# Kernel tuning notes

Measured on AMD Instinct MI355X. Metric: run time of the kernel, lower is better.

The kernel has to match this reference:

```python
import jax, jax.numpy as jnp
import numpy as np

K = 8   # heads
d = 8   # per-head dim
D = K * d  # 64


def setup_inputs() -> dict:
    key = jax.random.key(0)
    ks = jax.random.split(key, 12)
    B, T, N = 8, 12, 512
    s2 = 1.0 / np.sqrt(2 * D)
    s1 = 1.0 / np.sqrt(D)
    return {
        "X": jax.random.normal(ks[0], (B, T, N, D), jnp.float32),
        "STE": jax.random.normal(ks[1], (B, T, N, D), jnp.float32),
        "W7": jax.random.uniform(ks[2], (2 * D, D), jnp.float32, -s2, s2),
        "b7": jnp.zeros((D,), jnp.float32),
        "W8": jax.random.uniform(ks[3], (2 * D, D), jnp.float32, -s2, s2),
        "b8": jnp.zeros((D,), jnp.float32),
        "W9": jax.random.uniform(ks[4], (2 * D, D), jnp.float32, -s2, s2),
        "b9": jnp.zeros((D,), jnp.float32),
        "W10": jax.random.uniform(ks[5], (D, D), jnp.float32, -s1, s1),
        "b10": jnp.zeros((D,), jnp.float32),
        "W11": jax.random.uniform(ks[6], (D, D), jnp.float32, -s1, s1),
        "b11": jnp.zeros((D,), jnp.float32),
    }


def _heads(x):
    # torch.cat(torch.split(x, d, -1), 0): [B,T,N,D] -> [K,B,T,N,d] (head-major batch)
    B, T, N, _ = x.shape
    return jnp.moveaxis(x.reshape(B, T, N, K, d), 3, 0)


def reference(X, STE, W7, b7, W8, b8, W9, b9, W10, b10, W11, b11):
    H = jnp.concatenate([X, STE], axis=-1)                 # [B,T,N,2D]
    q = _heads(jax.nn.relu(H @ W7 + b7))                   # [K,B,T,N,d]
    k = _heads(jax.nn.relu(H @ W8 + b8))
    v = _heads(jax.nn.relu(H @ W9 + b9))
    scores = jnp.einsum('kbtnd,kbtmd->kbtnm', q, k) / jnp.sqrt(jnp.float32(d))
    attn = jax.nn.softmax(scores, axis=-1)                 # [K,B,T,N,N]
    out = jnp.einsum('kbtnm,kbtmd->kbtnd', attn, v)        # [K,B,T,N,d]
    # torch.cat(torch.split(out, B, 0), -1): [K,B,T,N,d] -> [B,T,N,K*d]
    Kk, B, T, N, _ = out.shape
    out = jnp.moveaxis(out, 0, 3).reshape(B, T, N, D)
    return jax.nn.relu(out @ W10 + b10) @ W11 + b11
```

## Files before the change

kernel.cpp:

```cpp
#include <hip/hip_runtime.h>
#include <hip/hip_bf16.h>
#include <math.h>

#define BT    96
#define NSEQ  512
#define DMODEL 64
#define RTOT  (BT * NSEQ)

#define QOFF  0
#define KOFF  ((size_t)RTOT * DMODEL)
#define VOFF  ((size_t)2 * RTOT * DMODEL)
#define OOFF  ((size_t)3 * RTOT * DMODEL)
#define WOFF  ((size_t)4 * RTOT * DMODEL)

static __device__ inline float fast_exp2(float x) {
#if __has_builtin(__builtin_amdgcn_exp2f)
    return __builtin_amdgcn_exp2f(x);
#else
    float r; asm("v_exp_f32 %0, %1" : "=v"(r) : "v"(x)); return r;
#endif
}
static __device__ inline float fast_rcp(float x) {
#if __has_builtin(__builtin_amdgcn_rcpf)
    return __builtin_amdgcn_rcpf(x);
#else
    return 1.f / x;
#endif
}

typedef __attribute__((ext_vector_type(8)))  short short8;
typedef __attribute__((ext_vector_type(16))) float float16v;

static __device__ inline short8 as_s8(uint4 u) {
    union { uint4 u; short8 s; } x; x.u = u; return x.s;
}

static __device__ inline uint32_t bf162_bits(__hip_bfloat162 h) {
    union { __hip_bfloat162 h; uint32_t u; } x; x.h = h; return x.u;
}

static __device__ inline void split_pack8(const float* v, uint4* hi, uint4* lo) {
    uint32_t h[4], l[4];
    #pragma unroll
    for (int t = 0; t < 4; ++t) {
        float x0 = v[2 * t], x1 = v[2 * t + 1];
        uint32_t hw = bf162_bits(__float22bfloat162_rn(make_float2(x0, x1)));
        float h0 = __uint_as_float(hw << 16);
        float h1 = __uint_as_float(hw & 0xffff0000u);
        h[t] = hw;
        float l0 = x0 - h0;
        float l1 = x1 - h1;
        l[t] = bf162_bits(__float22bfloat162_rn(make_float2(l0, l1)));
    }
    *hi = make_uint4(h[0], h[1], h[2], h[3]);
    *lo = make_uint4(l[0], l[1], l[2], l[3]);
}

__global__ __launch_bounds__(256) void wprep_kernel(
    const float* __restrict__ W7, const float* __restrict__ W8,
    const float* __restrict__ W9, const float* __restrict__ W10,
    const float* __restrict__ W11,
    uint4* __restrict__ WfH, uint4* __restrict__ WfL)
{
    const int e = blockIdx.x * 256 + threadIdx.x;
    const float* W;
    int k0, col;
    if (e < 3072) {
        int n  = e & 31;
        int t  = (e >> 5) & 1;
        int hh = (e >> 6) & 1;
        int c  = (e >> 7) & 7;
        int w  = e >> 10;
        W = (w == 0) ? W7 : (w == 1) ? W8 : W9;
        k0 = c * 16 + hh * 8;
        col = t * 32 + n;
    } else {
        int pe = e - 3072;
        int n  = pe & 31;
        int t  = (pe >> 5) & 1;
        int hh = (pe >> 6) & 1;
        int c  = (pe >> 7) & 3;
        int m  = pe >> 9;
        W = (m == 0) ? W10 : W11;
        k0 = c * 16 + hh * 8;
        col = t * 32 + n;
    }
    float v[8];
    #pragma unroll
    for (int j = 0; j < 8; ++j) v[j] = W[(size_t)(k0 + j) * 64 + col];
    uint4 hi, lo;
    split_pack8(v, &hi, &lo);
    WfH[e] = hi;
    WfL[e] = lo;
}

__global__ __launch_bounds__(384) void qkv_kernel(
    const float* __restrict__ X, const float* __restrict__ STE,
    const uint4* __restrict__ WfH, const uint4* __restrict__ WfL,
    const float* __restrict__ b7, const float* __restrict__ b8,
    const float* __restrict__ b9,
    float* __restrict__ qkv)
{
    __shared__ uint4 aH[512];
    __shared__ uint4 aL[512];

    const int tid  = threadIdx.x;
    const int l31  = tid & 31;
    const int hh   = (tid >> 5) & 1;
    const int wave = tid >> 6;
    const int w    = wave >> 1;
    const int tt   = wave & 1;
    const size_t blockrow = (size_t)blockIdx.x * 32;

    for (int e = tid; e < 512; e += 384) {
        const int el  = e & 31;
        const int ehh = (e >> 5) & 1;
        const int ec  = e >> 6;
        const float* src = (ec < 4) ? X : STE;
        const float* ap = src + (blockrow + el) * 64 + (ec & 3) * 16 + ehh * 8;
        float av[8];
        {
            float4 a0 = *(const float4*)(ap);
            float4 a1 = *(const float4*)(ap + 4);
            av[0] = a0.x; av[1] = a0.y; av[2] = a0.z; av[3] = a0.w;
            av[4] = a1.x; av[5] = a1.y; av[6] = a1.z; av[7] = a1.w;
        }
        uint4 hi, lo;
        split_pack8(av, &hi, &lo);
        aH[e] = hi;
        aL[e] = lo;
    }
    __syncthreads();

    float16v accM, accC;
    #pragma unroll
    for (int i = 0; i < 16; ++i) { accM[i] = 0.f; accC[i] = 0.f; }

    #pragma unroll
    for (int c = 0; c < 8; ++c) {
        const uint4 ahi = aH[c * 64 + hh * 32 + l31];
        const uint4 alo = aL[c * 64 + hh * 32 + l31];
        const int ei = w * 1024 + c * 128 + hh * 64 + tt * 32 + l31;
        const uint4 bh = WfH[ei];
        const uint4 bl = WfL[ei];
        accM = __builtin_amdgcn_mfma_f32_32x32x16_bf16(
            as_s8(ahi), as_s8(bh), accM, 0, 0, 0);
        accC = __builtin_amdgcn_mfma_f32_32x32x16_bf16(
            as_s8(alo), as_s8(bh), accC, 0, 0, 0);
        accC = __builtin_amdgcn_mfma_f32_32x32x16_bf16(
            as_s8(ahi), as_s8(bl), accC, 0, 0, 0);
    }

    const float* bv = (w == 0) ? b7 : (w == 1) ? b8 : b9;
    float* obase = qkv + (size_t)w * ((size_t)RTOT * DMODEL);
    const int col = tt * 32 + l31;
    const float bias = bv[col];
    #pragma unroll
    for (int r = 0; r < 16; ++r) {
        const int rowC = (r & 3) + 8 * (r >> 2) + 4 * hh;
        obase[(blockrow + rowC) * 64 + col] =
            fmaxf(accM[r] + accC[r] + bias, 0.f);
    }
}

__global__ __launch_bounds__(512, 4) void attn_kernel(
    const float* __restrict__ qkv, float* __restrict__ obuf)
{
    __shared__ uint4 ak1[16 * 32];
    __shared__ uint4 ak2p[16 * 33];
    __shared__ uint4 vfh[640];
    __shared__ uint4 vfl[640];

    const int tid  = threadIdx.x;
    const int lane = tid & 63;
    const int l31  = lane & 31;
    const int hh   = lane >> 5;
    const int wv   = tid >> 6;
    const int head = blockIdx.x & 7;
    const int bt   = blockIdx.x >> 3;

    const size_t rowbase = (size_t)bt * NSEQ * 64 + (size_t)head * 8;
    const float* Qp = qkv + QOFF + rowbase;
    const float* Kp = qkv + KOFF + rowbase;
    const float* Vp = qkv + VOFF + rowbase;

    const uint4 z4 = make_uint4(0, 0, 0, 0);

    {
        const int k = tid;
        const float* kr = Kp + (size_t)k * 64;
        float kv[8];
        float4 a = *(const float4*)(kr);
        float4 b = *(const float4*)(kr + 4);
        kv[0] = a.x; kv[1] = a.y; kv[2] = a.z; kv[3] = a.w;
        kv[4] = b.x; kv[5] = b.y; kv[6] = b.z; kv[7] = b.w;
        uint4 hi, lo;
        split_pack8(kv, &hi, &lo);
        ak1[k] = hi;
        ak2p[(k >> 5) * 33 + (k & 31)] = lo;
    }
    if (tid < 16) ak2p[tid * 33 + 32] = z4;

    for (int e = tid; e < 640; e += 512) {
        if (e < 576) {
            int s  = e / 18;
            int r  = e % 18;
            int hv = r / 9;
            int n  = r % 9;
            float vv[8];
            #pragma unroll
            for (int j = 0; j < 8; ++j) {
                int key = 16 * s + ((j < 4) ? (4 * hv + j) : (8 + 4 * hv + (j - 4)));
                vv[j] = (n < 8) ? Vp[(size_t)key * 64 + n] : 1.0f;
            }
            uint4 hi, lo;
            split_pack8(vv, &hi, &lo);
            vfh[e] = hi;
            vfl[e] = lo;
        } else {
            vfh[e] = z4;
            vfl[e] = z4;
        }
    }

    __syncthreads();

    const float C = 0.51012091684045906f;
    const int idx2 = hh ? 32 : l31;

    float16v Z16;
    #pragma unroll
    for (int i = 0; i < 16; ++i) Z16[i] = 0.f;

    for (int qt = wv; qt < 16; qt += 8) {
        const float* qp = Qp + (size_t)(qt * 32 + l31) * 64;
        float qv[8];
        {
            float4 a = *(const float4*)(qp);
            float4 b = *(const float4*)(qp + 4);
            qv[0] = a.x * C; qv[1] = a.y * C; qv[2] = a.z * C; qv[3] = a.w * C;
            qv[4] = b.x * C; qv[5] = b.y * C; qv[6] = b.z * C; qv[7] = b.w * C;
        }
        uint4 qhi, qlo;
        split_pack8(qv, &qhi, &qlo);
        const uint4 bq1 = hh ? qlo : qhi;
        const uint4 bq2 = qhi;

        float16v Oa = Z16, Ob = Z16;

        float16v S0;
        {
            const uint4 a1 = ak1[l31];
            const uint4 a2 = ak2p[idx2];
            S0 = __builtin_amdgcn_mfma_f32_32x32x16_bf16(as_s8(a1), as_s8(bq1), Z16, 0, 0, 0);
            S0 = __builtin_amdgcn_mfma_f32_32x32x16_bf16(as_s8(a2), as_s8(bq2), S0, 0, 0, 0);
        }

        #pragma unroll 2
        for (int c = 0; c < 16; ++c) {
            const int cn = (c + 1) & 15;
            const int vi0 = (4 * c + hh) * 9;
            const int vi1 = (4 * c + 2 + hh) * 9;
            const uint4 bh0 = vfh[vi0 + l31];
            const uint4 bl0 = vfl[vi0 + l31];
            const uint4 bh1 = vfh[vi1 + l31];
            const uint4 bl1 = vfl[vi1 + l31];

            const uint4 a1n = ak1[cn * 32 + l31];
            const uint4 a2n = ak2p[cn * 33 + idx2];
            float16v S1;
            S1 = __builtin_amdgcn_mfma_f32_32x32x16_bf16(as_s8(a1n), as_s8(bq1), Z16, 0, 0, 0);
            S1 = __builtin_amdgcn_mfma_f32_32x32x16_bf16(as_s8(a2n), as_s8(bq2), S1, 0, 0, 0);

            #pragma unroll
            for (int i = 0; i < 16; ++i) S0[i] = fast_exp2(S0[i]);

            float pv[16];
            #pragma unroll
            for (int i = 0; i < 16; ++i) pv[i] = S0[i];
            uint4 ph0, pl0, ph1, pl1;
            split_pack8(&pv[0], &ph0, &pl0);
            split_pack8(&pv[8], &ph1, &pl1);

            Oa = __builtin_amdgcn_mfma_f32_32x32x16_bf16(as_s8(ph0), as_s8(bh0), Oa, 0, 0, 0);
            Ob = __builtin_amdgcn_mfma_f32_32x32x16_bf16(as_s8(ph1), as_s8(bh1), Ob, 0, 0, 0);
            Oa = __builtin_amdgcn_mfma_f32_32x32x16_bf16(as_s8(pl0), as_s8(bh0), Oa, 0, 0, 0);
            Ob = __builtin_amdgcn_mfma_f32_32x32x16_bf16(as_s8(pl1), as_s8(bh1), Ob, 0, 0, 0);
            Oa = __builtin_amdgcn_mfma_f32_32x32x16_bf16(as_s8(ph0), as_s8(bl0), Oa, 0, 0, 0);
            Ob = __builtin_amdgcn_mfma_f32_32x32x16_bf16(as_s8(ph1), as_s8(bl1), Ob, 0, 0, 0);

            S0 = S1;
        }

        #pragma unroll
        for (int r = 0; r < 16; ++r) {
            float ov = Oa[r] + Ob[r];
            float den = __uint_as_float(
                __builtin_amdgcn_ds_swizzle(__float_as_uint(ov), 0x100));
            float o = ov * fast_rcp(den);
            if (l31 < 8) {
                int row = (r & 3) + 8 * (r >> 2) + 4 * hh;
                obuf[rowbase + (size_t)(qt * 32 + row) * 64 + l31] = o;
            }
        }
    }
}

__global__ __launch_bounds__(128) void proj_kernel(
    const float* __restrict__ obuf,
    const uint4* __restrict__ WfH, const uint4* __restrict__ WfL,
    const float* __restrict__ b10, const float* __restrict__ b11,
    float* __restrict__ out)
{
    __shared__ float Ts[32][80];

    const int tid  = threadIdx.x;
    const int lane = tid & 63;
    const int l31  = lane & 31;
    const int hh   = lane >> 5;
    const int tw   = tid >> 6;
    const size_t row = (size_t)blockIdx.x * 32 + l31;
    const size_t blockrow = (size_t)blockIdx.x * 32;

    float16v accM, accC;
    #pragma unroll
    for (int i = 0; i < 16; ++i) { accM[i] = 0.f; accC[i] = 0.f; }

    #pragma unroll
    for (int c = 0; c < 4; ++c) {
        const float* ap = obuf + row * 64 + c * 16 + hh * 8;
        float av[8];
        {
            float4 a0 = *(const float4*)(ap);
            float4 a1 = *(const float4*)(ap + 4);
            av[0] = a0.x; av[1] = a0.y; av[2] = a0.z; av[3] = a0.w;
            av[4] = a1.x; av[5] = a1.y; av[6] = a1.z; av[7] = a1.w;
        }
        uint4 ahi, alo;
        split_pack8(av, &ahi, &alo);

        const int ei = 3072 + c * 128 + hh * 64 + tw * 32 + l31;
        const uint4 bh = WfH[ei];
        const uint4 bl = WfL[ei];
        accM = __builtin_amdgcn_mfma_f32_32x32x16_bf16(
            as_s8(ahi), as_s8(bh), accM, 0, 0, 0);
        accC = __builtin_amdgcn_mfma_f32_32x32x16_bf16(
            as_s8(alo), as_s8(bh), accC, 0, 0, 0);
        accC = __builtin_amdgcn_mfma_f32_32x32x16_bf16(
            as_s8(ahi), as_s8(bl), accC, 0, 0, 0);
    }

    {
        const int col = tw * 32 + l31;
        const float bias = b10[col];
        #pragma unroll
        for (int r = 0; r < 16; ++r) {
            const int rowC = (r & 3) + 8 * (r >> 2) + 4 * hh;
            Ts[rowC][col] = fmaxf(accM[r] + accC[r] + bias, 0.f);
        }
    }
    __syncthreads();

    #pragma unroll
    for (int i = 0; i < 16; ++i) { accM[i] = 0.f; accC[i] = 0.f; }

    #pragma unroll
    for (int c = 0; c < 4; ++c) {
        const float* ap = &Ts[l31][c * 16 + hh * 8];
        float av[8];
        {
            float4 a0 = *(const float4*)(ap);
            float4 a1 = *(const float4*)(ap + 4);
            av[0] = a0.x; av[1] = a0.y; av[2] = a0.z; av[3] = a0.w;
            av[4] = a1.x; av[5] = a1.y; av[6] = a1.z; av[7] = a1.w;
        }
        uint4 ahi, alo;
        split_pack8(av, &ahi, &alo);

        const int ei = 3584 + c * 128 + hh * 64 + tw * 32 + l31;
        const uint4 bh = WfH[ei];
        const uint4 bl = WfL[ei];
        accM = __builtin_amdgcn_mfma_f32_32x32x16_bf16(
            as_s8(ahi), as_s8(bh), accM, 0, 0, 0);
        accC = __builtin_amdgcn_mfma_f32_32x32x16_bf16(
            as_s8(alo), as_s8(bh), accC, 0, 0, 0);
        accC = __builtin_amdgcn_mfma_f32_32x32x16_bf16(
            as_s8(ahi), as_s8(bl), accC, 0, 0, 0);
    }

    {
        const int col = tw * 32 + l31;
        const float bias = b11[col];
        #pragma unroll
        for (int r = 0; r < 16; ++r) {
            const int rowC = (r & 3) + 8 * (r >> 2) + 4 * hh;
            out[(blockrow + rowC) * 64 + col] = accM[r] + accC[r] + bias;
        }
    }
}

extern "C" void kernel_launch(void* const* d_in, const int* in_sizes, int n_in,
                              void* d_out, int out_size, void* d_ws, size_t ws_size,
                              hipStream_t stream)
{
    const float* X   = (const float*)d_in[0];
    const float* STE = (const float*)d_in[1];
    const float* W7  = (const float*)d_in[2];
    const float* b7  = (const float*)d_in[3];
    const float* W8  = (const float*)d_in[4];
    const float* b8  = (const float*)d_in[5];
    const float* W9  = (const float*)d_in[6];
    const float* b9  = (const float*)d_in[7];
    const float* W10 = (const float*)d_in[8];
    const float* b10 = (const float*)d_in[9];
    const float* W11 = (const float*)d_in[10];
    const float* b11 = (const float*)d_in[11];

    float* ws  = (float*)d_ws;
    float* out = (float*)d_out;

    uint4* WfH = (uint4*)(ws + WOFF);
    uint4* WfL = WfH + 4096;

    wprep_kernel<<<dim3(16), 256, 0, stream>>>(W7, W8, W9, W10, W11, WfH, WfL);
    qkv_kernel<<<dim3(RTOT / 32), 384, 0, stream>>>(X, STE, WfH, WfL, b7, b8, b9, ws);
    attn_kernel<<<dim3(BT * 8), 512, 0, stream>>>(ws, ws + OOFF);
    proj_kernel<<<dim3(RTOT / 32), 128, 0, stream>>>(ws + OOFF, WfH, WfL, b10, b11, out);
}
```

Measured before the change: 180.0 us.

## Store Q/K/V/O in head-major planes and simplify attention loop pipelining

The QKV projection now writes outputs in head-major planes ([head][row][8]), so attention blocks read each head's Q, K and V as contiguous 32-byte rows instead of strided 8-float slices. The attention output buffer and the projection kernel's loads are changed to match. The QKV kernel first stages the X/STE rows through a padded shared-memory tile using coalesced float4 loads. The attention loop's manual software pipelining, where the next S tile was computed ahead and unrolled by 2, is removed in favour of a simpler sequential loop. This may lose MFMA/exp overlap and adds some extra shared memory in the QKV kernel.

Measured after the change: 173.8 us. 3.4% less time.

```diff
diff --git a/kernel.cpp b/kernel.cpp
--- a/kernel.cpp
+++ b/kernel.cpp
@@ -12,6 +12,8 @@
 #define VOFF  ((size_t)2 * RTOT * DMODEL)
 #define OOFF  ((size_t)3 * RTOT * DMODEL)
 #define WOFF  ((size_t)4 * RTOT * DMODEL)
+
+#define HPLANE ((size_t)RTOT * 8)
 
 static __device__ inline float fast_exp2(float x) {
 #if __has_builtin(__builtin_amdgcn_exp2f)
@@ -101,6 +103,7 @@
     const float* __restrict__ b9,
     float* __restrict__ qkv)
 {
+    __shared__ float Xs[32][132];
     __shared__ uint4 aH[512];
     __shared__ uint4 aL[512];
 
@@ -112,19 +115,24 @@
     const int tt   = wave & 1;
     const size_t blockrow = (size_t)blockIdx.x * 32;
 
+    for (int e = tid; e < 1024; e += 384) {
+        const int row = e >> 5;
+        const int seg = e & 31;
+        const float* src = (seg < 16) ? X : STE;
+        const float4 v = *(const float4*)(src + (blockrow + row) * 64 + (seg & 15) * 4);
+        float* dst = &Xs[row][seg * 4];
+        dst[0] = v.x; dst[1] = v.y; dst[2] = v.z; dst[3] = v.w;
+    }
+    __syncthreads();
+
     for (int e = tid; e < 512; e += 384) {
         const int el  = e & 31;
         const int ehh = (e >> 5) & 1;
         const int ec  = e >> 6;
-        const float* src = (ec < 4) ? X : STE;
-        const float* ap = src + (blockrow + el) * 64 + (ec & 3) * 16 + ehh * 8;
+        const float* hp = &Xs[el][ec * 16 + ehh * 8];
         float av[8];
-        {
-            float4 a0 = *(const float4*)(ap);
-            float4 a1 = *(const float4*)(ap + 4);
-            av[0] = a0.x; av[1] = a0.y; av[2] = a0.z; av[3] = a0.w;
-            av[4] = a1.x; av[5] = a1.y; av[6] = a1.z; av[7] = a1.w;
-        }
+        #pragma unroll
+        for (int j = 0; j < 8; ++j) av[j] = hp[j];
         uint4 hi, lo;
         split_pack8(av, &hi, &lo);
         aH[e] = hi;
@@ -152,13 +160,15 @@
     }
 
     const float* bv = (w == 0) ? b7 : (w == 1) ? b8 : b9;
-    float* obase = qkv + (size_t)w * ((size_t)RTOT * DMODEL);
-    const int col = tt * 32 + l31;
+    const int head = tt * 4 + (l31 >> 3);
+    const int d    = l31 & 7;
+    const int col  = tt * 32 + l31;
+    float* obase = qkv + (size_t)w * ((size_t)RTOT * DMODEL) + (size_t)head * HPLANE;
     const float bias = bv[col];
     #pragma unroll
     for (int r = 0; r < 16; ++r) {
         const int rowC = (r & 3) + 8 * (r >> 2) + 4 * hh;
-        obase[(blockrow + rowC) * 64 + col] =
+        obase[(blockrow + rowC) * 8 + d] =
             fmaxf(accM[r] + accC[r] + bias, 0.f);
     }
 }
@@ -179,16 +189,16 @@
     const int head = blockIdx.x & 7;
     const int bt   = blockIdx.x >> 3;
 
-    const size_t rowbase = (size_t)bt * NSEQ * 64 + (size_t)head * 8;
-    const float* Qp = qkv + QOFF + rowbase;
-    const float* Kp = qkv + KOFF + rowbase;
-    const float* Vp = qkv + VOFF + rowbase;
+    const size_t hb = (size_t)head * HPLANE + (size_t)bt * (NSEQ * 8);
+    const float* Qp = qkv + QOFF + hb;
+    const float* Kp = qkv + KOFF + hb;
+    const float* Vp = qkv + VOFF + hb;
 
     const uint4 z4 = make_uint4(0, 0, 0, 0);
 
     {
         const int k = tid;
-        const float* kr = Kp + (size_t)k * 64;
+        const float* kr = Kp + (size_t)k * 8;
         float kv[8];
         float4 a = *(const float4*)(kr);
         float4 b = *(const float4*)(kr + 4);
@@ -211,7 +221,7 @@
             #pragma unroll
             for (int j = 0; j < 8; ++j) {
                 int key = 16 * s + ((j < 4) ? (4 * hv + j) : (8 + 4 * hv + (j - 4)));
-                vv[j] = (n < 8) ? Vp[(size_t)key * 64 + n] : 1.0f;
+                vv[j] = (n < 8) ? Vp[(size_t)key * 8 + n] : 1.0f;
             }
             uint4 hi, lo;
             split_pack8(vv, &hi, &lo);
@@ -233,7 +243,7 @@
     for (int i = 0; i < 16; ++i) Z16[i] = 0.f;
 
     for (int qt = wv; qt < 16; qt += 8) {
-        const float* qp = Qp + (size_t)(qt * 32 + l31) * 64;
+        const float* qp = Qp + (size_t)(qt * 32 + l31) * 8;
         float qv[8];
         {
             float4 a = *(const float4*)(qp);
@@ -248,48 +258,35 @@
 
         float16v Oa = Z16, Ob = Z16;
 
-        float16v S0;
-        {
-            const uint4 a1 = ak1[l31];
-            const uint4 a2 = ak2p[idx2];
-            S0 = __builtin_amdgcn_mfma_f32_32x32x16_bf16(as_s8(a1), as_s8(bq1), Z16, 0, 0, 0);
-            S0 = __builtin_amdgcn_mfma_f32_32x32x16_bf16(as_s8(a2), as_s8(bq2), S0, 0, 0, 0);
-        }
-
-        #pragma unroll 2
         for (int c = 0; c < 16; ++c) {
-            const int cn = (c + 1) & 15;
-            const int vi0 = (4 * c + hh) * 9;
-            const int vi1 = (4 * c + 2 + hh) * 9;
-            const uint4 bh0 = vfh[vi0 + l31];
-            const uint4 bl0 = vfl[vi0 + l31];
-            const uint4 bh1 = vfh[vi1 + l31];
-            const uint4 bl1 = vfl[vi1 + l31];
-
-            const uint4 a1n = ak1[cn * 32 + l31];
-            const uint4 a2n = ak2p[cn * 33 + idx2];
-            float16v S1;
-            S1 = __builtin_amdgcn_mfma_f32_32x32x16_bf16(as_s8(a1n), as_s8(bq1), Z16, 0, 0, 0);
-            S1 = __builtin_amdgcn_mfma_f32_32x32x16_bf16(as_s8(a2n), as_s8(bq2), S1, 0, 0, 0);
-
-            #pragma unroll
-            for (int i = 0; i < 16; ++i) S0[i] = fast_exp2(S0[i]);
+            const uint4 a1 = ak1[c * 32 + l31];
+            const uint4 a2 = ak2p[c * 33 + idx2];
+
+            float16v S;
+            S = __builtin_amdgcn_mfma_f32_32x32x16_bf16(as_s8(a1), as_s8(bq1), Z16, 0, 0, 0);
+            S = __builtin_amdgcn_mfma_f32_32x32x16_bf16(as_s8(a2), as_s8(bq2), S, 0, 0, 0);
 
             float pv[16];
             #pragma unroll
-            for (int i = 0; i < 16; ++i) pv[i] = S0[i];
+            for (int i = 0; i < 16; ++i) pv[i] = fast_exp2(S[i]);
+
             uint4 ph0, pl0, ph1, pl1;
             split_pack8(&pv[0], &ph0, &pl0);
             split_pack8(&pv[8], &ph1, &pl1);
 
+            const int vi0 = (4 * c + hh) * 9;
+            const uint4 bh0 = vfh[vi0 + l31];
+            const uint4 bl0 = vfl[vi0 + l31];
             Oa = __builtin_amdgcn_mfma_f32_32x32x16_bf16(as_s8(ph0), as_s8(bh0), Oa, 0, 0, 0);
+            Oa = __builtin_amdgcn_mfma_f32_32x32x16_bf16(as_s8(pl0), as_s8(bh0), Oa, 0, 0, 0);
+            Oa = __builtin_amdgcn_mfma_f32_32x32x16_bf16(as_s8(ph0), as_s8(bl0), Oa, 0, 0, 0);
+
+            const int vi1 = (4 * c + 2 + hh) * 9;
+            const uint4 bh1 = vfh[vi1 + l31];
+            const uint4 bl1 = vfl[vi1 + l31];
             Ob = __builtin_amdgcn_mfma_f32_32x32x16_bf16(as_s8(ph1), as_s8(bh1), Ob, 0, 0, 0);
-            Oa = __builtin_amdgcn_mfma_f32_32x32x16_bf16(as_s8(pl0), as_s8(bh0), Oa, 0, 0, 0);
             Ob = __builtin_amdgcn_mfma_f32_32x32x16_bf16(as_s8(pl1), as_s8(bh1), Ob, 0, 0, 0);
-            Oa = __builtin_amdgcn_mfma_f32_32x32x16_bf16(as_s8(ph0), as_s8(bl0), Oa, 0, 0, 0);
             Ob = __builtin_amdgcn_mfma_f32_32x32x16_bf16(as_s8(ph1), as_s8(bl1), Ob, 0, 0, 0);
-
-            S0 = S1;
         }
 
         #pragma unroll
@@ -300,7 +297,7 @@
             float o = ov * fast_rcp(den);
             if (l31 < 8) {
                 int row = (r & 3) + 8 * (r >> 2) + 4 * hh;
-                obuf[rowbase + (size_t)(qt * 32 + row) * 64 + l31] = o;
+                obuf[hb + (size_t)(qt * 32 + row) * 8 + l31] = o;
             }
         }
     }
@@ -328,7 +325,7 @@
 
     #pragma unroll
     for (int c = 0; c < 4; ++c) {
-        const float* ap = obuf + row * 64 + c * 16 + hh * 8;
+        const float* ap = obuf + (size_t)(2 * c + hh) * HPLANE + row * 8;
         float av[8];
         {
             float4 a0 = *(const float4*)(ap);
```
